# Kernel tuning notes

Hardware: AMD Instinct MI355X
Metric: run time of the kernel (lower is better)

The kernel has to match this reference:

```python
import jax, jax.numpy as jnp
import numpy as np

N_NODES = 50000
N_EDGES = 800000
D_IN = 256
D_OUT = 256
HEADS = (4, 4)
NEG_SLOPE = 0.2


def gat_conv(x, W, attn_l, attn_r, bias, src, dst, n_nodes, apply_elu):
    """DGL GATConv forward (no dropout, eval mode).
    x: [N, F_in], W: [F_in, H*D], attn_l/attn_r: [H, D], bias: [H*D].
    Returns [N, H, D].
    """
    H, D = attn_l.shape
    feat = (x @ W).reshape(n_nodes, H, D)                      # [N,H,D]
    el = jnp.einsum('nhd,hd->nh', feat, attn_l)                # [N,H]
    er = jnp.einsum('nhd,hd->nh', feat, attn_r)                # [N,H]
    e = jax.nn.leaky_relu(el[src] + er[dst], NEG_SLOPE)        # [E,H]
    # edge softmax over incoming edges of each dst node
    m = jax.ops.segment_max(e, dst, num_segments=n_nodes)      # [N,H]
    ex = jnp.exp(e - m[dst])                                   # [E,H]
    denom = jax.ops.segment_sum(ex, dst, num_segments=n_nodes) # [N,H]
    alpha = ex / denom[dst]                                    # [E,H]
    msg = feat[src] * alpha[..., None]                         # [E,H,D]
    out = jax.ops.segment_sum(msg, dst, num_segments=n_nodes)  # [N,H,D]
    out = out + bias.reshape(1, H, D)
    if apply_elu:
        out = jax.nn.elu(out)
    return out


def setup_inputs() -> dict:
    key = jax.random.key(0)
    ks = jax.random.split(key, 12)
    H1, H2 = HEADS
    D1 = D_OUT // H1
    D2 = D_OUT // H2
    x = jax.random.normal(ks[0], (N_NODES, D_IN), dtype=jnp.float32)
    src = jax.random.randint(ks[1], (N_EDGES,), 0, N_NODES, dtype=jnp.int32)
    dst = jax.random.randint(ks[2], (N_EDGES,), 0, N_NODES, dtype=jnp.int32)
    s1 = 1.0 / np.sqrt(D_IN)
    s2 = 1.0 / np.sqrt(D_OUT)
    W1 = jax.random.normal(ks[3], (D_IN, H1 * D1), dtype=jnp.float32) * s1
    al1 = jax.random.normal(ks[4], (H1, D1), dtype=jnp.float32) * s2
    ar1 = jax.random.normal(ks[5], (H1, D1), dtype=jnp.float32) * s2
    b1 = jnp.zeros((H1 * D1,), dtype=jnp.float32)
    W2 = jax.random.normal(ks[6], (D_OUT, H2 * D2), dtype=jnp.float32) * s2
    al2 = jax.random.normal(ks[7], (H2, D2), dtype=jnp.float32) * s2
    ar2 = jax.random.normal(ks[8], (H2, D2), dtype=jnp.float32) * s2
    b2 = jnp.zeros((H2 * D2,), dtype=jnp.float32)
    return {"x": x, "src": src, "dst": dst,
            "W1": W1, "al1": al1, "ar1": ar1, "b1": b1,
            "W2": W2, "al2": al2, "ar2": ar2, "b2": b2}


def reference(x, src, dst, W1, al1, ar1, b1, W2, al2, ar2, b2):
    h1 = gat_conv(x, W1, al1, ar1, b1, src, dst, N_NODES, apply_elu=True)
    h1 = h1.reshape(N_NODES, -1)                               # [N, 256]
    h2 = gat_conv(h1, W2, al2, ar2, b2, src, dst, N_NODES, apply_elu=False)
    h2 = h2.reshape(N_NODES, -1)                               # [N, 256]
    return jnp.concatenate([x, h1, h2], axis=1)                # [N, 768]
```

## Files before the change

### kernel.cpp

```cpp
#include <hip/hip_runtime.h>
#include <hip/hip_bf16.h>

#define N_NODES 50000
#define N_EDGES 800000
#define HEADS 4
#define FDIM 256
#define OUT_STRIDE 768
#define SCAN_B 256
#define NBLK ((N_NODES + SCAN_B - 1) / SCAN_B)

typedef __attribute__((ext_vector_type(8))) short short8;
typedef __attribute__((ext_vector_type(4))) float f32x4;

__device__ __forceinline__ float lrelu(float v) { return v > 0.f ? v : 0.2f * v; }

__device__ __forceinline__ unsigned short f2bf(float f) {
    unsigned u = __float_as_uint(f);
    return (unsigned short)((u + 0x7fffu + ((u >> 16) & 1u)) >> 16);
}
__device__ __forceinline__ float bf2f(unsigned short s) {
    return __uint_as_float(((unsigned)s) << 16);
}

__global__ void k_copy_x(const float* __restrict__ x, float* __restrict__ out) {
    int idx = blockIdx.x * blockDim.x + threadIdx.x;
    if (idx >= N_NODES * 64) return;
    int n = idx >> 6, q = idx & 63;
    float4 v = *(const float4*)&x[(size_t)n * FDIM + q * 4];
    *(float4*)&out[(size_t)n * OUT_STRIDE + q * 4] = v;
}

__global__ void k_convW(const float* __restrict__ W,
                        unsigned short* __restrict__ bt_hi,
                        unsigned short* __restrict__ bt_lo) {
    int t = blockIdx.x * blockDim.x + threadIdx.x;
    int k = t >> 8, col = t & 255;
    float f = W[k * 256 + col];
    unsigned short h = f2bf(f);
    bt_hi[(size_t)col * 256 + k] = h;
    bt_lo[(size_t)col * 256 + k] = f2bf(f - bf2f(h));
}

__device__ __forceinline__ int a_idx(int row, int cq) {
    return row * 256 + ((cq ^ (row & 31)) << 3);
}

__global__ __launch_bounds__(512) void k_gemm_mfma(
        const float* __restrict__ A, int lda,
        const unsigned short* __restrict__ bt_hi, const unsigned short* __restrict__ bt_lo,
        float* __restrict__ C, int M,
        const float* __restrict__ al, const float* __restrict__ ar,
        float* __restrict__ el, float* __restrict__ er) {
    __shared__ __align__(16) unsigned short As_hi[64 * 256];
    __shared__ __align__(16) unsigned short As_lo[64 * 256];
    const int tid = threadIdx.x;
    const int brow = blockIdx.x * 64;

    {
        const int row = tid >> 3;
        const int seg = tid & 7;
        const int grow = brow + row;
        const bool valid = grow < M;
        const float* ap = A + (size_t)grow * lda + seg * 32;
#pragma unroll
        for (int c = 0; c < 4; ++c) {
            float fv[8];
            if (valid) {
                float4 f0 = *(const float4*)(ap + c * 8);
                float4 f1 = *(const float4*)(ap + c * 8 + 4);
                fv[0]=f0.x; fv[1]=f0.y; fv[2]=f0.z; fv[3]=f0.w;
                fv[4]=f1.x; fv[5]=f1.y; fv[6]=f1.z; fv[7]=f1.w;
            } else {
#pragma unroll
                for (int j = 0; j < 8; ++j) fv[j] = 0.f;
            }
            short8 vh, vl;
#pragma unroll
            for (int j = 0; j < 8; ++j) {
                unsigned short h = f2bf(fv[j]);
                vh[j] = (short)h;
                vl[j] = (short)f2bf(fv[j] - bf2f(h));
            }
            int idx = a_idx(row, seg * 4 + c);
            *(short8*)&As_hi[idx] = vh;
            *(short8*)&As_lo[idx] = vl;
        }
    }
    __syncthreads();

    const int lane = tid & 63;
    const int w = tid >> 6;
    const int wr = w >> 2;
    const int wc = w & 3;
    const int ln15 = lane & 15;
    const int kg = lane >> 4;
    f32x4 acc[2][4] = {};

#pragma unroll 2
    for (int ks = 0; ks < 8; ++ks) {
        short8 ah[2], am[2];
#pragma unroll
        for (int rf = 0; rf < 2; ++rf) {
            int idx = a_idx(wr * 32 + rf * 16 + ln15, ks * 4 + kg);
            ah[rf] = *(const short8*)&As_hi[idx];
            am[rf] = *(const short8*)&As_lo[idx];
        }
#pragma unroll
        for (int cf = 0; cf < 4; ++cf) {
            size_t boff = (size_t)(wc * 64 + cf * 16 + ln15) * 256 + ks * 32 + kg * 8;
            short8 bh = *(const short8*)&bt_hi[boff];
            short8 bl = *(const short8*)&bt_lo[boff];
#pragma unroll
            for (int rf = 0; rf < 2; ++rf) {
                acc[rf][cf] = __builtin_amdgcn_mfma_f32_16x16x32_bf16(ah[rf], bh, acc[rf][cf], 0, 0, 0);
                acc[rf][cf] = __builtin_amdgcn_mfma_f32_16x16x32_bf16(am[rf], bh, acc[rf][cf], 0, 0, 0);
                acc[rf][cf] = __builtin_amdgcn_mfma_f32_16x16x32_bf16(ah[rf], bl, acc[rf][cf], 0, 0, 0);
            }
        }
    }

#pragma unroll
    for (int rf = 0; rf < 2; ++rf) {
        float pel[4] = {0.f, 0.f, 0.f, 0.f};
        float per[4] = {0.f, 0.f, 0.f, 0.f};
#pragma unroll
        for (int cf = 0; cf < 4; ++cf) {
            int gcol = wc * 64 + cf * 16 + ln15;
            float alv = al[gcol], arv = ar[gcol];
#pragma unroll
            for (int reg = 0; reg < 4; ++reg) {
                float v = acc[rf][cf][reg];
                int gr = brow + wr * 32 + rf * 16 + kg * 4 + reg;
                if (gr < M) C[(size_t)gr * 256 + gcol] = v;
                pel[reg] += v * alv;
                per[reg] += v * arv;
            }
        }
#pragma unroll
        for (int reg = 0; reg < 4; ++reg) {
#pragma unroll
            for (int off = 1; off <= 8; off <<= 1) {
                pel[reg] += __shfl_xor(pel[reg], off, 64);
                per[reg] += __shfl_xor(per[reg], off, 64);
            }
        }
        if (ln15 == 0) {
#pragma unroll
            for (int reg = 0; reg < 4; ++reg) {
                int gr = brow + wr * 32 + rf * 16 + kg * 4 + reg;
                if (gr < M) {
                    el[gr * HEADS + wc] = pel[reg];
                    er[gr * HEADS + wc] = per[reg];
                }
            }
        }
    }
}

__global__ void k_zero_counts(int* __restrict__ counts) {
    int i = blockIdx.x * blockDim.x + threadIdx.x;
    if (i < N_NODES) counts[i] = 0;
}
__global__ void k_hist(const int* __restrict__ dst, int* __restrict__ counts) {
    int e = blockIdx.x * blockDim.x + threadIdx.x;
    if (e < N_EDGES) atomicAdd(&counts[dst[e]], 1);
}
__global__ void k_scan1(const int* __restrict__ counts, int* __restrict__ excl,
                        int* __restrict__ blocksums) {
    __shared__ int s[SCAN_B];
    int tid = threadIdx.x;
    int i = blockIdx.x * SCAN_B + tid;
    int v = (i < N_NODES) ? counts[i] : 0;
    s[tid] = v;
    __syncthreads();
    for (int off = 1; off < SCAN_B; off <<= 1) {
        int t = (tid >= off) ? s[tid - off] : 0;
        __syncthreads();
        s[tid] += t;
        __syncthreads();
    }
    if (i < N_NODES) excl[i] = s[tid] - v;
    if (tid == SCAN_B - 1) blocksums[blockIdx.x] = s[tid];
}
__global__ void k_scan2(int* __restrict__ blocksums) {
    __shared__ int s[SCAN_B];
    int tid = threadIdx.x;
    int v = (tid < NBLK) ? blocksums[tid] : 0;
    s[tid] = v;
    __syncthreads();
    for (int off = 1; off < SCAN_B; off <<= 1) {
        int t = (tid >= off) ? s[tid - off] : 0;
        __syncthreads();
        s[tid] += t;
        __syncthreads();
    }
    if (tid < NBLK) blocksums[tid] = s[tid] - v;
}
__global__ void k_scan3(const int* __restrict__ excl, const int* __restrict__ blocksums,
                        int* __restrict__ row_start, int* __restrict__ cursor) {
    int i = blockIdx.x * blockDim.x + threadIdx.x;
    if (i >= N_NODES) return;
    int r = excl[i] + blocksums[i >> 8];
    row_start[i] = r;
    cursor[i] = r;
}
__global__ void k_place(const int* __restrict__ src, const int* __restrict__ dst,
                        int* __restrict__ cursor, int* __restrict__ csr_src) {
    int e = blockIdx.x * blockDim.x + threadIdx.x;
    if (e >= N_EDGES) return;
    int pos = atomicAdd(&cursor[dst[e]], 1);
    csr_src[pos] = src[e];
}

__global__ void k_gather(const int* __restrict__ row_start, const int* __restrict__ counts,
                         const int* __restrict__ csr_src,
                         const float* __restrict__ feat,
                         const float* __restrict__ el, const float* __restrict__ er,
                         const float* __restrict__ bias,
                         float* __restrict__ out_slice, int apply_elu) {
    int gtid = blockIdx.x * blockDim.x + threadIdx.x;
    int node = gtid >> 6;
    if (node >= N_NODES) return;
    int lane = threadIdx.x & 63;
    int h = lane >> 4;
    float4 bv = *(const float4*)&bias[lane * 4];
    int start = row_start[node];
    int cnt = counts[node];
    float4 acc = make_float4(0.f, 0.f, 0.f, 0.f);
    if (cnt > 0) {
        float erd = er[node * HEADS + h];
        float m = -1e30f, denom = 0.f;
        for (int i = 0; i < cnt; ++i) {
            int s = csr_src[start + i];
            float v = lrelu(el[s * HEADS + h] + erd);
            float mn = fmaxf(m, v);
            float scale = __expf(m - mn);
            float ex = __expf(v - mn);
            m = mn;
            denom = denom * scale + ex;
            float4 f = *(const float4*)&feat[(size_t)s * FDIM + lane * 4];
            acc.x = acc.x * scale + ex * f.x;
            acc.y = acc.y * scale + ex * f.y;
            acc.z = acc.z * scale + ex * f.z;
            acc.w = acc.w * scale + ex * f.w;
        }
        float inv = 1.f / denom;
        acc.x = acc.x * inv + bv.x; acc.y = acc.y * inv + bv.y;
        acc.z = acc.z * inv + bv.z; acc.w = acc.w * inv + bv.w;
    } else {
        acc = bv;
    }
    if (apply_elu) {
        acc.x = acc.x > 0.f ? acc.x : expm1f(acc.x);
        acc.y = acc.y > 0.f ? acc.y : expm1f(acc.y);
        acc.z = acc.z > 0.f ? acc.z : expm1f(acc.z);
        acc.w = acc.w > 0.f ? acc.w : expm1f(acc.w);
    }
    *(float4*)&out_slice[(size_t)node * OUT_STRIDE + lane * 4] = acc;
}

static void run_layer(const float* in, int lda,
                      const float* W, const float* al, const float* ar, const float* bias,
                      float* out_slice, int apply_elu,
                      const int* row_start, const int* counts, const int* csr_src,
                      float* feat, float* el, float* er,
                      unsigned short* bt_hi, unsigned short* bt_lo, hipStream_t stream) {
    k_convW<<<256, 256, 0, stream>>>(W, bt_hi, bt_lo);
    k_gemm_mfma<<<(N_NODES + 63) / 64, 512, 0, stream>>>(
        in, lda, bt_hi, bt_lo, feat, N_NODES, al, ar, el, er);
    k_gather<<<(N_NODES * 64 + 255) / 256, 256, 0, stream>>>(
        row_start, counts, csr_src, feat, el, er, bias, out_slice, apply_elu);
}

extern "C" void kernel_launch(void* const* d_in, const int* in_sizes, int n_in,
                              void* d_out, int out_size, void* d_ws, size_t ws_size,
                              hipStream_t stream) {
    const float* x   = (const float*)d_in[0];
    const int*   src = (const int*)d_in[1];
    const int*   dst = (const int*)d_in[2];
    const float* W1  = (const float*)d_in[3];
    const float* al1 = (const float*)d_in[4];
    const float* ar1 = (const float*)d_in[5];
    const float* b1  = (const float*)d_in[6];
    const float* W2  = (const float*)d_in[7];
    const float* al2 = (const float*)d_in[8];
    const float* ar2 = (const float*)d_in[9];
    const float* b2  = (const float*)d_in[10];
    float* out = (float*)d_out;

    size_t need_bytes = ((size_t)N_NODES * FDIM + 2u * N_NODES * HEADS) * 4u
                      + ((size_t)4 * N_NODES + 256 + N_EDGES) * 4u
                      + 2u * 65536u * 2u;
    if (ws_size < need_bytes) return;

    float* ws        = (float*)d_ws;
    float* feat      = ws;
    float* el        = feat + (size_t)N_NODES * FDIM;
    float* er        = el + N_NODES * HEADS;
    int*   counts    = (int*)(er + N_NODES * HEADS);
    int*   excl      = counts + N_NODES;
    int*   row_start = excl + N_NODES;
    int*   cursor    = row_start + N_NODES;
    int*   blocksums = cursor + N_NODES;
    int*   csr_src   = blocksums + 256;
    unsigned short* bt_hi = (unsigned short*)(csr_src + N_EDGES);
    unsigned short* bt_lo = bt_hi + 65536;

    k_zero_counts<<<(N_NODES + 255) / 256, 256, 0, stream>>>(counts);
    k_hist<<<(N_EDGES + 255) / 256, 256, 0, stream>>>(dst, counts);
    k_scan1<<<NBLK, SCAN_B, 0, stream>>>(counts, excl, blocksums);
    k_scan2<<<1, SCAN_B, 0, stream>>>(blocksums);
    k_scan3<<<(N_NODES + 255) / 256, 256, 0, stream>>>(excl, blocksums, row_start, cursor);
    k_place<<<(N_EDGES + 255) / 256, 256, 0, stream>>>(src, dst, cursor, csr_src);

    k_copy_x<<<(N_NODES * 64 + 255) / 256, 256, 0, stream>>>(x, out);

    run_layer(x, FDIM, W1, al1, ar1, b1, out + 256, 1,
              row_start, counts, csr_src, feat, el, er, bt_hi, bt_lo, stream);

    run_layer(out + 256, OUT_STRIDE, W2, al2, ar2, b2, out + 512, 0,
              row_start, counts, csr_src, feat, el, er, bt_hi, bt_lo, stream);
}
```

Measured before the change: 712.0 us.

## Store projected features as fp16 and fuse x copy into first GEMM

The projected node features are now written as fp16 instead of fp32, which halves the bytes the edge-gather kernel reads per source node. Attention logits el/er are still computed from the fp32 accumulators. The separate kernel that copied x into the output is removed, and the first-layer GEMM writes x to the output while loading its A tile. This trades feature precision (fp16 rounding of the messages) for lower gather bandwidth and one fewer launch.

After: 695.1 us. 2.4% less time.

```diff
diff --git a/kernel.cpp b/kernel.cpp
--- a/kernel.cpp
+++ b/kernel.cpp
@@ -1,5 +1,6 @@
 #include <hip/hip_runtime.h>
 #include <hip/hip_bf16.h>
+#include <hip/hip_fp16.h>
 
 #define N_NODES 50000
 #define N_EDGES 800000
@@ -20,14 +21,6 @@
 }
 __device__ __forceinline__ float bf2f(unsigned short s) {
     return __uint_as_float(((unsigned)s) << 16);
-}
-
-__global__ void k_copy_x(const float* __restrict__ x, float* __restrict__ out) {
-    int idx = blockIdx.x * blockDim.x + threadIdx.x;
-    if (idx >= N_NODES * 64) return;
-    int n = idx >> 6, q = idx & 63;
-    float4 v = *(const float4*)&x[(size_t)n * FDIM + q * 4];
-    *(float4*)&out[(size_t)n * OUT_STRIDE + q * 4] = v;
 }
 
 __global__ void k_convW(const float* __restrict__ W,
@@ -48,9 +41,10 @@
 __global__ __launch_bounds__(512) void k_gemm_mfma(
         const float* __restrict__ A, int lda,
         const unsigned short* __restrict__ bt_hi, const unsigned short* __restrict__ bt_lo,
-        float* __restrict__ C, int M,
+        __half* __restrict__ feat, int M,
         const float* __restrict__ al, const float* __restrict__ ar,
-        float* __restrict__ el, float* __restrict__ er) {
+        float* __restrict__ el, float* __restrict__ er,
+        float* __restrict__ xcopy) {
     __shared__ __align__(16) unsigned short As_hi[64 * 256];
     __shared__ __align__(16) unsigned short As_lo[64 * 256];
     const int tid = threadIdx.x;
@@ -70,6 +64,11 @@
                 float4 f1 = *(const float4*)(ap + c * 8 + 4);
                 fv[0]=f0.x; fv[1]=f0.y; fv[2]=f0.z; fv[3]=f0.w;
                 fv[4]=f1.x; fv[5]=f1.y; fv[6]=f1.z; fv[7]=f1.w;
+                if (xcopy) {
+                    float* xp = &xcopy[(size_t)grow * OUT_STRIDE + seg * 32 + c * 8];
+                    *(float4*)xp = f0;
+                    *(float4*)(xp + 4) = f1;
+                }
             } else {
 #pragma unroll
                 for (int j = 0; j < 8; ++j) fv[j] = 0.f;
@@ -131,7 +130,7 @@
             for (int reg = 0; reg < 4; ++reg) {
                 float v = acc[rf][cf][reg];
                 int gr = brow + wr * 32 + rf * 16 + kg * 4 + reg;
-                if (gr < M) C[(size_t)gr * 256 + gcol] = v;
+                if (gr < M) feat[(size_t)gr * 256 + gcol] = __float2half(v);
                 pel[reg] += v * alv;
                 per[reg] += v * arv;
             }
@@ -214,7 +213,7 @@
 
 __global__ void k_gather(const int* __restrict__ row_start, const int* __restrict__ counts,
                          const int* __restrict__ csr_src,
-                         const float* __restrict__ feat,
+                         const __half* __restrict__ feat,
                          const float* __restrict__ el, const float* __restrict__ er,
                          const float* __restrict__ bias,
                          float* __restrict__ out_slice, int apply_elu) {
@@ -238,11 +237,15 @@
             float ex = __expf(v - mn);
             m = mn;
             denom = denom * scale + ex;
-            float4 f = *(const float4*)&feat[(size_t)s * FDIM + lane * 4];
-            acc.x = acc.x * scale + ex * f.x;
-            acc.y = acc.y * scale + ex * f.y;
-            acc.z = acc.z * scale + ex * f.z;
-            acc.w = acc.w * scale + ex * f.w;
+            uint2 raw = *(const uint2*)&feat[(size_t)s * FDIM + lane * 4];
+            __half2 p0 = *(__half2*)&raw.x;
+            __half2 p1 = *(__half2*)&raw.y;
+            float2 f0 = __half22float2(p0);
+            float2 f1 = __half22float2(p1);
+            acc.x = acc.x * scale + ex * f0.x;
+            acc.y = acc.y * scale + ex * f0.y;
+            acc.z = acc.z * scale + ex * f1.x;
+            acc.w = acc.w * scale + ex * f1.y;
         }
         float inv = 1.f / denom;
         acc.x = acc.x * inv + bv.x; acc.y = acc.y * inv + bv.y;
@@ -261,13 +264,13 @@
 
 static void run_layer(const float* in, int lda,
                       const float* W, const float* al, const float* ar, const float* bias,
-                      float* out_slice, int apply_elu,
+                      float* out_slice, int apply_elu, float* xcopy,
                       const int* row_start, const int* counts, const int* csr_src,
-                      float* feat, float* el, float* er,
+                      __half* feat, float* el, float* er,
                       unsigned short* bt_hi, unsigned short* bt_lo, hipStream_t stream) {
     k_convW<<<256, 256, 0, stream>>>(W, bt_hi, bt_lo);
     k_gemm_mfma<<<(N_NODES + 63) / 64, 512, 0, stream>>>(
-        in, lda, bt_hi, bt_lo, feat, N_NODES, al, ar, el, er);
+        in, lda, bt_hi, bt_lo, feat, N_NODES, al, ar, el, er, xcopy);
     k_gather<<<(N_NODES * 64 + 255) / 256, 256, 0, stream>>>(
         row_start, counts, csr_src, feat, el, er, bias, out_slice, apply_elu);
 }
@@ -288,14 +291,14 @@
     const float* b2  = (const float*)d_in[10];
     float* out = (float*)d_out;
 
-    size_t need_bytes = ((size_t)N_NODES * FDIM + 2u * N_NODES * HEADS) * 4u
+    size_t need_bytes = ((size_t)N_NODES * 128 + 2u * N_NODES * HEADS) * 4u
                       + ((size_t)4 * N_NODES + 256 + N_EDGES) * 4u
                       + 2u * 65536u * 2u;
     if (ws_size < need_bytes) return;
 
     float* ws        = (float*)d_ws;
-    float* feat      = ws;
-    float* el        = feat + (size_t)N_NODES * FDIM;
+    __half* feat     = (__half*)ws;
+    float* el        = ws + (size_t)N_NODES * 128;
     float* er        = el + N_NODES * HEADS;
     int*   counts    = (int*)(er + N_NODES * HEADS);
     int*   excl      = counts + N_NODES;
@@ -313,11 +316,9 @@
     k_scan3<<<(N_NODES + 255) / 256, 256, 0, stream>>>(excl, blocksums, row_start, cursor);
     k_place<<<(N_EDGES + 255) / 256, 256, 0, stream>>>(src, dst, cursor, csr_src);
 
-    k_copy_x<<<(N_NODES * 64 + 255) / 256, 256, 0, stream>>>(x, out);
-
-    run_layer(x, FDIM, W1, al1, ar1, b1, out + 256, 1,
+    run_layer(x, FDIM, W1, al1, ar1, b1, out + 256, 1, out,
               row_start, counts, csr_src, feat, el, er, bt_hi, bt_lo, stream);
 
-    run_layer(out + 256, OUT_STRIDE, W2, al2, ar2, b2, out + 512, 0,
+    run_layer(out + 256, OUT_STRIDE, W2, al2, ar2, b2, out + 512, 0, nullptr,
               row_start, counts, csr_src, feat, el, er, bt_hi, bt_lo, stream);
 }
```
